# Performance work log

Measured on AMD Instinct MI355X. Metric: run time of the kernel, lower is better.

## Reference

```python
import jax, jax.numpy as jnp
import numpy as np

N, T, V, C = 16, 288, 25, 128
S, W = 8, 3            # num_subset, temporal window
IC = C // S            # inter_channels = 16
EPS = 1e-5


def _bn(x, g, b, m, v):
    # eval-mode BatchNorm2d over channel axis 1 of (N,C,T,V)
    inv = jax.lax.rsqrt(v + EPS)
    return (x - m[:, None, None]) * (inv * g)[:, None, None] + b[:, None, None]


def _conv1x1(x, w, b):
    # x: (N,Cin,T,V), w: (Cout,Cin), b: (Cout,)
    return jnp.einsum('nctv,oc->notv', x, w) + b[:, None, None]


def setup_inputs() -> dict:
    key = jax.random.key(0)
    ks = jax.random.split(key, 16)
    rn = lambda k, s, sc=0.05: jax.random.normal(k, s, dtype=jnp.float32) * sc
    inp = {
        'x': jax.random.normal(ks[0], (N, T, V, C), dtype=jnp.float32),
        'w_k': rn(ks[1], (S * IC, C)), 'b_k': rn(ks[2], (S * IC,)),
        'w_q': rn(ks[3], (S * IC, C)), 'b_q': rn(ks[4], (S * IC,)),
        'alphas': jnp.ones((1, S, 1, 1), jnp.float32),
        'att0': jnp.ones((1, S, W * V, V), jnp.float32) / V,
        'w_out': rn(ks[5], (C, S * C)), 'b_out': rn(ks[6], (C,)),
        'g_out': jnp.ones((C,), jnp.float32), 'beta_out': jnp.zeros((C,), jnp.float32),
        'm_out': jnp.zeros((C,), jnp.float32), 'v_out': jnp.ones((C,), jnp.float32),
        'w_ff': rn(ks[7], (C, C)), 'b_ff': rn(ks[8], (C,)),
        'g_ff': jnp.ones((C,), jnp.float32), 'beta_ff': jnp.zeros((C,), jnp.float32),
        'm_ff': jnp.zeros((C,), jnp.float32), 'v_ff': jnp.ones((C,), jnp.float32),
        'w_t': rn(ks[9], (C, C, 7, 1)), 'b_t': rn(ks[10], (C,)),
        'g_t': jnp.ones((C,), jnp.float32), 'beta_t': jnp.zeros((C,), jnp.float32),
        'm_t': jnp.zeros((C,), jnp.float32), 'v_t': jnp.ones((C,), jnp.float32),
    }
    return inp


def reference(x, w_k, b_k, w_q, b_q, alphas, att0,
              w_out, b_out, g_out, beta_out, m_out, v_out,
              w_ff, b_ff, g_ff, beta_ff, m_ff, v_ff,
              w_t, b_t, g_t, beta_t, m_t, v_t):
    leaky = lambda a: jax.nn.leaky_relu(a, 0.1)
    xc = jnp.transpose(x, (0, 3, 1, 2))                 # (N,C,T,V)
    # UnfoldTemporalWindows(window=3, stride=1, dilation=1, pad=1)
    xp = jnp.pad(xc, ((0, 0), (0, 0), (1, 1), (0, 0)))
    up = jnp.stack([xp[:, :, i:i + T] for i in range(W)], axis=3)   # (N,C,T,W,V)
    up = up.reshape(N, C, T, W * V)                      # (N,C,T,W*V)

    k = _conv1x1(xc, w_k, b_k).reshape(N, S, IC, T, V)
    q = _conv1x1(up, w_q, b_q).reshape(N, S, IC, T, W * V)
    scores = jnp.einsum('nsctu,nsctv->nsuv', q, k) / (IC * T)
    attention = jax.nn.softmax(scores, axis=-2) * alphas + att0      # atts buffer is zeros

    y = jnp.einsum('nctu,nsuv->nsctv', up, attention).reshape(N, S * C, T, V)
    y = _bn(_conv1x1(y, w_out, b_out), g_out, beta_out, m_out, v_out)
    y = leaky(xc + y)                                    # downs1 = identity (Cin==Cout)
    y = _bn(_conv1x1(y, w_ff, b_ff), g_ff, beta_ff, m_ff, v_ff)
    y = leaky(xc + y)                                    # downs2 = identity

    z = jax.lax.conv_general_dilated(
        y, w_t, window_strides=(1, 1), padding=((3, 3), (0, 0)),
        dimension_numbers=('NCHW', 'OIHW', 'NCHW')) + b_t[None, :, None, None]
    z = _bn(z, g_t, beta_t, m_t, v_t)
    z = leaky(y + z)                                     # downt2 = identity
    z = jax.nn.relu(z + xc)                              # residual add of identity
    return jnp.transpose(z, (0, 2, 3, 1))                # (N,T,V,C)
```

## Files before the change

### kernel.cpp

```cpp
#include <hip/hip_runtime.h>


#define NN 16
#define TT 288
#define VV 25
#define CC 128
#define SS 8
#define UU 75
#define TP 290
#define EPSF 1e-5f

typedef __attribute__((ext_vector_type(8))) short bf16x8;
typedef __attribute__((ext_vector_type(4))) float f32x4;

static __device__ __forceinline__ ushort f2bf(float f) {
  uint u = __float_as_uint(f);
  u = (u + 0x7FFFu + ((u >> 16) & 1u)) >> 16;
  return (ushort)u;
}

__global__ __launch_bounds__(256) void k_wcvt(
    const float* __restrict__ w_out, const float* __restrict__ w_k,
    const float* __restrict__ w_q, const float* __restrict__ w_ff,
    ushort* __restrict__ wb, ushort* __restrict__ wkqb,
    ushort* __restrict__ wffb) {
  int i = blockIdx.x * 256 + threadIdx.x;
  if (i < 131072) {
    int j = i >> 7, c = i & 127;
    int s = j >> 7, o = j & 127;
    wb[i] = f2bf(w_out[(o << 10) + (s << 7) + c]);
  } else {
    int j = i - 131072;
    if (j < 16384) wkqb[j] = f2bf(w_k[j]);
    else if (j < 32768) wkqb[j] = f2bf(w_q[j - 16384]);
    else wffb[j - 32768] = f2bf(w_ff[j - 32768]);
  }
}

__global__ __launch_bounds__(256) void k_qkg(
    const float* __restrict__ x, const ushort* __restrict__ wkqb,
    const float* __restrict__ b_k, const float* __restrict__ b_q,
    ushort* __restrict__ kb, ushort* __restrict__ qb) {
  __shared__ __align__(16) ushort As[8][128][8];
  __shared__ __align__(16) ushort Bs[8][128][8];
  const int bm = blockIdx.x, by = blockIdx.y;
  const int gm0 = bm << 7;
  const int tid = threadIdx.x;
  const int lane = tid & 63, wid = tid >> 6;
  const int wm = wid >> 1, wn = wid & 1;
  const int srow = tid & 127;
  const int skg0 = tid >> 7;
  const ushort* wsrc = wkqb + by * 16384;
  f32x4 acc[4][4] = {};
  for (int kh = 0; kh < 2; ++kh) {
    __syncthreads();
#pragma unroll
    for (int j = 0; j < 4; ++j) {
      int kg = skg0 + 2 * j;
      const float* xp = x + (((size_t)(gm0 + srow)) << 7) + kh * 64 + kg * 8;
      float4 a0 = *(const float4*)xp;
      float4 a1 = *(const float4*)(xp + 4);
      uint4 pk;
      pk.x = (uint)f2bf(a0.x) | ((uint)f2bf(a0.y) << 16);
      pk.y = (uint)f2bf(a0.z) | ((uint)f2bf(a0.w) << 16);
      pk.z = (uint)f2bf(a1.x) | ((uint)f2bf(a1.y) << 16);
      pk.w = (uint)f2bf(a1.z) | ((uint)f2bf(a1.w) << 16);
      *(uint4*)&As[kg][srow][0] = pk;
      *(uint4*)&Bs[kg][srow][0] =
          *(const uint4*)&wsrc[(srow << 7) + kh * 64 + kg * 8];
    }
    __syncthreads();
#pragma unroll
    for (int ks = 0; ks < 2; ++ks) {
      int g = ks * 4 + (lane >> 4);
      bf16x8 af[4], bfr[4];
#pragma unroll
      for (int mi = 0; mi < 4; ++mi)
        af[mi] = *(const bf16x8*)&As[g][wm * 64 + mi * 16 + (lane & 15)][0];
#pragma unroll
      for (int ni = 0; ni < 4; ++ni)
        bfr[ni] = *(const bf16x8*)&Bs[g][wn * 64 + ni * 16 + (lane & 15)][0];
#pragma unroll
      for (int mi = 0; mi < 4; ++mi)
#pragma unroll
        for (int ni = 0; ni < 4; ++ni)
          acc[mi][ni] = __builtin_amdgcn_mfma_f32_16x16x32_bf16(
              af[mi], bfr[ni], acc[mi][ni], 0, 0, 0);
    }
  }
  const int l15 = lane & 15, l4 = lane >> 4;
  const float* bias = by ? b_q : b_k;
#pragma unroll
  for (int ni = 0; ni < 4; ++ni) {
    int col = wn * 64 + ni * 16 + l15;
    float bb = bias[col];
#pragma unroll
    for (int mi = 0; mi < 4; ++mi) {
#pragma unroll
      for (int reg = 0; reg < 4; ++reg) {
        int row = gm0 + wm * 64 + mi * 16 + (l4 << 2) + reg;
        ushort val = f2bf(acc[mi][ni][reg] + bb);
        if (by == 0) {
          kb[((size_t)row << 7) + col] = val;
        } else {
          int n = row / 7200;
          qb[((size_t)(row + n * 50 + 25) << 7) + col] = val;
        }
      }
    }
  }
}

__global__ __launch_bounds__(256) void k_qkpad(const float* __restrict__ b_q,
                                               ushort* __restrict__ qb) {
  int i = blockIdx.x * 256 + threadIdx.x;
  int o = i & 127;
  int r = i >> 7;
  int v = r % 25;
  int e = (r / 25) & 1;
  int n = r / 50;
  int tp = e ? 289 : 0;
  qb[((size_t)((n * TP + tp) * VV + v) << 7) + o] = f2bf(b_q[o]);
}

__global__ __launch_bounds__(512) void k_scores(
    const ushort* __restrict__ kb, const ushort* __restrict__ qb,
    const float* __restrict__ alphas, const float* __restrict__ att0,
    ushort* __restrict__ attTb) {
  __shared__ float red[8][2640];
  __shared__ float scl[1875];
  __shared__ float mx[25];
  __shared__ float den[25];
  const int bx = blockIdx.x;
  const int n = bx >> 3, s = bx & 7;
  const int tid = threadIdx.x;
  const int lane = tid & 63, wid = tid >> 6;
  const int l15 = lane & 15, l4 = lane >> 4;
  const int dt = l4 >> 1;
  const int sic = s * 16 + (l4 & 1) * 8;
  int qoff[5];
#pragma unroll
  for (int tu = 0; tu < 5; ++tu) {
    int u = tu * 16 + l15;
    int w = u / 25, vp = u - w * 25;
    qoff[tu] = (w * 25 + vp) * 128 + sic;
  }
  const bool qv4 = (64 + l15) < 75;
  const bool kv1 = (16 + l15) < 25;
  int koff0 = l15 * 128 + sic;
  int koff1 = (16 + l15) * 128 + sic;
  const ushort* qbase = qb + (size_t)n * 928000 + (size_t)dt * 3200;
  const ushort* kbase = kb + (size_t)n * 921600 + (size_t)dt * 3200;
  f32x4 acc[5][2] = {};
  const bf16x8 zf = {};
  for (int kk = wid; kk < 144; kk += 8) {
    const ushort* qp = qbase + kk * 6400;
    const ushort* kp = kbase + kk * 6400;
    bf16x8 a[5], b[2];
#pragma unroll
    for (int tu = 0; tu < 4; ++tu) a[tu] = *(const bf16x8*)(qp + qoff[tu]);
    a[4] = qv4 ? *(const bf16x8*)(qp + qoff[4]) : zf;
    b[0] = *(const bf16x8*)(kp + koff0);
    b[1] = kv1 ? *(const bf16x8*)(kp + koff1) : zf;
#pragma unroll
    for (int tu = 0; tu < 5; ++tu)
#pragma unroll
      for (int tv = 0; tv < 2; ++tv)
        acc[tu][tv] = __builtin_amdgcn_mfma_f32_16x16x32_bf16(
            a[tu], b[tv], acc[tu][tv], 0, 0, 0);
  }
#pragma unroll
  for (int tu = 0; tu < 5; ++tu)
#pragma unroll
    for (int tv = 0; tv < 2; ++tv) {
#pragma unroll
      for (int reg = 0; reg < 4; ++reg)
        red[wid][(tu * 16 + l4 * 4 + reg) * 33 + tv * 16 + l15] =
            acc[tu][tv][reg];
    }
  __syncthreads();
  const float inv = 1.0f / 4608.0f;
  for (int i = tid; i < 1875; i += 512) {
    int u = i / 25, v = i - u * 25;
    float a = 0.f;
#pragma unroll
    for (int w = 0; w < 8; ++w) a += red[w][u * 33 + v];
    scl[i] = a * inv;
  }
  __syncthreads();
  if (tid < 25) {
    float m = -1e30f;
    for (int u = 0; u < 75; ++u) m = fmaxf(m, scl[u * 25 + tid]);
    float d = 0.f;
    for (int u = 0; u < 75; ++u) d += expf(scl[u * 25 + tid] - m);
    mx[tid] = m;
    den[tid] = d;
  }
  __syncthreads();
  const float alpha = alphas[s];
  ushort* op = attTb + (size_t)bx * 2400;
  for (int i = tid; i < 2400; i += 512) {
    int v = i / 96, u = i - v * 96;
    int w = u >> 5, vp = u & 31;
    float val = 0.f;
    if (vp < 25) {
      int uo = w * 25 + vp;
      val = expf(scl[uo * 25 + v] - mx[v]) / den[v] * alpha +
            att0[(s * 75 + uo) * 25 + v];
    }
    op[i] = f2bf(val);
  }
}

__global__ __launch_bounds__(256, 3) void k_attn3(
    const float* __restrict__ x, const ushort* __restrict__ attTb,
    const ushort* __restrict__ wb, const float* __restrict__ b_out,
    const float* __restrict__ g_out, const float* __restrict__ beta_out,
    const float* __restrict__ m_out, const float* __restrict__ v_out,
    float* __restrict__ y1) {
  __shared__ __align__(16) uint4 Xt4[128 * 16];
  __shared__ __align__(16) ushort Yl[2][32 * 136];
  const int t0 = blockIdx.x * 2, n = blockIdx.y;
  const int tid = threadIdx.x;
  for (int i = tid; i < 2048; i += 256) {
    int c = i & 127, chunk = i >> 7;
    int r = chunk >> 2, vp0 = (chunk & 3) * 8;
    int tr = t0 + r - 1;
    bool valid = (tr >= 0 && tr < TT);
    const float* xr = x + (((size_t)(n * TT + tr) * VV)) * 128 + c;
    float f[8];
#pragma unroll
    for (int j = 0; j < 8; ++j) {
      int vp = vp0 + j;
      f[j] = (valid && vp < 25) ? xr[vp * 128] : 0.f;
    }
    uint4 pk;
    pk.x = (uint)f2bf(f[0]) | ((uint)f2bf(f[1]) << 16);
    pk.y = (uint)f2bf(f[2]) | ((uint)f2bf(f[3]) << 16);
    pk.z = (uint)f2bf(f[4]) | ((uint)f2bf(f[5]) << 16);
    pk.w = (uint)f2bf(f[6]) | ((uint)f2bf(f[7]) << 16);
    Xt4[c * 16 + (chunk ^ (c & 7))] = pk;
  }
  __syncthreads();
  const int lane = tid & 63, wid = tid >> 6;
  const int l15 = lane & 15, l4 = lane >> 4;
  const bf16x8 zf = {};
  f32x4 accO[2][2][2] = {};
  const ushort* Avn = attTb + (size_t)n * 19200;
  const int c0r = wid * 32 + l15, c1r = wid * 32 + 16 + l15;
  for (int s = 0; s < 8; ++s) {
    const ushort* AvS = Avn + s * 2400;
    f32x4 accY[2][2][2] = {};
#pragma unroll
    for (int ks = 0; ks < 3; ++ks) {
      int u0 = ks * 32 + l4 * 8;
      bf16x8 av0 = *(const bf16x8*)&AvS[l15 * 96 + u0];
      int r1 = 16 + l15;
      bf16x8 av1 = *(const bf16x8*)&AvS[(r1 <= 24 ? r1 : 24) * 96 + u0];
      if (l15 > 8) av1 = zf;
#pragma unroll
      for (int tt = 0; tt < 2; ++tt) {
        int ch = (tt + ks) * 4 + l4;
        bf16x8 xb0 = *(const bf16x8*)&Xt4[c0r * 16 + (ch ^ (c0r & 7))];
        bf16x8 xb1 = *(const bf16x8*)&Xt4[c1r * 16 + (ch ^ (c1r & 7))];
        accY[tt][0][0] = __builtin_amdgcn_mfma_f32_16x16x32_bf16(av0, xb0, accY[tt][0][0], 0, 0, 0);
        accY[tt][0][1] = __builtin_amdgcn_mfma_f32_16x16x32_bf16(av0, xb1, accY[tt][0][1], 0, 0, 0);
        accY[tt][1][0] = __builtin_amdgcn_mfma_f32_16x16x32_bf16(av1, xb0, accY[tt][1][0], 0, 0, 0);
        accY[tt][1][1] = __builtin_amdgcn_mfma_f32_16x16x32_bf16(av1, xb1, accY[tt][1][1], 0, 0, 0);
      }
    }
    __syncthreads();
#pragma unroll
    for (int tt = 0; tt < 2; ++tt)
#pragma unroll
      for (int mi = 0; mi < 2; ++mi)
#pragma unroll
        for (int nj = 0; nj < 2; ++nj)
#pragma unroll
          for (int reg = 0; reg < 4; ++reg)
            Yl[tt][(mi * 16 + l4 * 4 + reg) * 136 + wid * 32 + nj * 16 + l15] =
                f2bf(accY[tt][mi][nj][reg]);
    __syncthreads();
    const ushort* wS = wb + s * 16384;
#pragma unroll
    for (int kc = 0; kc < 4; ++kc) {
      int c0 = kc * 32 + l4 * 8;
      bf16x8 wf0 = *(const bf16x8*)&wS[(wid * 32 + l15) * 128 + c0];
      bf16x8 wf1 = *(const bf16x8*)&wS[(wid * 32 + 16 + l15) * 128 + c0];
#pragma unroll
      for (int tt = 0; tt < 2; ++tt) {
        bf16x8 yb0 = *(const bf16x8*)&Yl[tt][l15 * 136 + c0];
        bf16x8 yb1 = *(const bf16x8*)&Yl[tt][(16 + l15) * 136 + c0];
        accO[tt][0][0] = __builtin_amdgcn_mfma_f32_16x16x32_bf16(wf0, yb0, accO[tt][0][0], 0, 0, 0);
        accO[tt][0][1] = __builtin_amdgcn_mfma_f32_16x16x32_bf16(wf0, yb1, accO[tt][0][1], 0, 0, 0);
        accO[tt][1][0] = __builtin_amdgcn_mfma_f32_16x16x32_bf16(wf1, yb0, accO[tt][1][0], 0, 0, 0);
        accO[tt][1][1] = __builtin_amdgcn_mfma_f32_16x16x32_bf16(wf1, yb1, accO[tt][1][1], 0, 0, 0);
      }
    }
  }
#pragma unroll
  for (int tt = 0; tt < 2; ++tt) {
    int t = t0 + tt;
#pragma unroll
    for (int nj = 0; nj < 2; ++nj) {
      int v = nj * 16 + l15;
      if (v < 25) {
        size_t rowbase = (((size_t)(n * TT + t) * VV + v)) * 128 + wid * 32;
#pragma unroll
        for (int mi = 0; mi < 2; ++mi) {
          int ob = mi * 16 + (l4 << 2);
          int og = wid * 32 + ob;
          float4 gg = *(const float4*)&g_out[og];
          float4 vv = *(const float4*)&v_out[og];
          float4 mm = *(const float4*)&m_out[og];
          float4 be = *(const float4*)&beta_out[og];
          float4 bo = *(const float4*)&b_out[og];
          float4 xv = *(const float4*)&x[rowbase + ob];
          float4 r;
          float s1, a;
          s1 = gg.x * rsqrtf(vv.x + EPSF);
          a = (accO[tt][mi][nj][0] + bo.x) * s1 + (be.x - mm.x * s1) + xv.x;
          r.x = a > 0.f ? a : 0.1f * a;
          s1 = gg.y * rsqrtf(vv.y + EPSF);
          a = (accO[tt][mi][nj][1] + bo.y) * s1 + (be.y - mm.y * s1) + xv.y;
          r.y = a > 0.f ? a : 0.1f * a;
          s1 = gg.z * rsqrtf(vv.z + EPSF);
          a = (accO[tt][mi][nj][2] + bo.z) * s1 + (be.z - mm.z * s1) + xv.z;
          r.z = a > 0.f ? a : 0.1f * a;
          s1 = gg.w * rsqrtf(vv.w + EPSF);
          a = (accO[tt][mi][nj][3] + bo.w) * s1 + (be.w - mm.w * s1) + xv.w;
          r.w = a > 0.f ? a : 0.1f * a;
          *(float4*)&y1[rowbase + ob] = r;
        }
      }
    }
  }
}

__global__ __launch_bounds__(256) void k_ffg(
    const float* __restrict__ y1, const float* __restrict__ x,
    const ushort* __restrict__ wffb, const float* __restrict__ b_ff,
    const float* __restrict__ g_ff, const float* __restrict__ beta_ff,
    const float* __restrict__ m_ff, const float* __restrict__ v_ff,
    float* __restrict__ y2) {
  __shared__ __align__(16) ushort As[8][128][8];
  __shared__ __align__(16) ushort Bs[8][128][8];
  const int gm0 = blockIdx.x << 7;
  const int tid = threadIdx.x;
  const int lane = tid & 63, wid = tid >> 6;
  const int wm = wid >> 1, wn = wid & 1;
  const int srow = tid & 127;
  const int skg0 = tid >> 7;
  f32x4 acc[4][4] = {};
  for (int kh = 0; kh < 2; ++kh) {
    __syncthreads();
#pragma unroll
    for (int j = 0; j < 4; ++j) {
      int kg = skg0 + 2 * j;
      const float* yp = y1 + (((size_t)(gm0 + srow)) << 7) + kh * 64 + kg * 8;
      float4 a0 = *(const float4*)yp;
      float4 a1 = *(const float4*)(yp + 4);
      uint4 pk;
      pk.x = (uint)f2bf(a0.x) | ((uint)f2bf(a0.y) << 16);
      pk.y = (uint)f2bf(a0.z) | ((uint)f2bf(a0.w) << 16);
      pk.z = (uint)f2bf(a1.x) | ((uint)f2bf(a1.y) << 16);
      pk.w = (uint)f2bf(a1.z) | ((uint)f2bf(a1.w) << 16);
      *(uint4*)&As[kg][srow][0] = pk;
      *(uint4*)&Bs[kg][srow][0] =
          *(const uint4*)&wffb[(srow << 7) + kh * 64 + kg * 8];
    }
    __syncthreads();
#pragma unroll
    for (int ks = 0; ks < 2; ++ks) {
      int g = ks * 4 + (lane >> 4);
      bf16x8 af[4], bfr[4];
#pragma unroll
      for (int mi = 0; mi < 4; ++mi)
        af[mi] = *(const bf16x8*)&As[g][wm * 64 + mi * 16 + (lane & 15)][0];
#pragma unroll
      for (int ni = 0; ni < 4; ++ni)
        bfr[ni] = *(const bf16x8*)&Bs[g][wn * 64 + ni * 16 + (lane & 15)][0];
#pragma unroll
      for (int mi = 0; mi < 4; ++mi)
#pragma unroll
        for (int ni = 0; ni < 4; ++ni)
          acc[mi][ni] = __builtin_amdgcn_mfma_f32_16x16x32_bf16(
              af[mi], bfr[ni], acc[mi][ni], 0, 0, 0);
    }
  }
  const int l15 = lane & 15, l4 = lane >> 4;
#pragma unroll
  for (int ni = 0; ni < 4; ++ni) {
    int o = wn * 64 + ni * 16 + l15;
    float s1 = g_ff[o] * rsqrtf(v_ff[o] + EPSF);
    float sh = beta_ff[o] - m_ff[o] * s1;
    float bb = b_ff[o];
#pragma unroll
    for (int mi = 0; mi < 4; ++mi) {
#pragma unroll
      for (int reg = 0; reg < 4; ++reg) {
        int row = gm0 + wm * 64 + mi * 16 + (l4 << 2) + reg;
        size_t idx = ((size_t)row << 7) + o;
        float a = (acc[mi][ni][reg] + bb) * s1 + sh;
        float rr = x[idx] + a;
        y2[idx] = rr > 0.f ? rr : 0.1f * rr;
      }
    }
  }
}

__global__ __launch_bounds__(256) void k_wtb(const float* __restrict__ w_t,
                                             ushort* __restrict__ wbt) {
  int i = blockIdx.x * 256 + threadIdx.x;
  if (i < 128 * 128 * 7) {
    int o = i / 896;
    int rem = i - o * 896;
    int c = rem / 7, kt = rem - c * 7;
    wbt[o * 896 + kt * 128 + c] = f2bf(w_t[i]);
  }
}

__global__ __launch_bounds__(256, 2) void k_tconv(
    const float* __restrict__ y2, const float* __restrict__ x,
    const ushort* __restrict__ wbt, const float* __restrict__ b_t,
    const float* __restrict__ g_t, const float* __restrict__ beta_t,
    const float* __restrict__ m_t, const float* __restrict__ v_t,
    float* __restrict__ out) {
  __shared__ __align__(16) uint4 As[280 * 16];
  const int n = blockIdx.y;
  const int r0 = blockIdx.x << 7;
  const int tid = threadIdx.x;
  const float* y2n = y2 + ((size_t)n * 7200 << 7);
  for (int i = tid; i < 278 * 16; i += 256) {
    int rl = i >> 4, cc = i & 15;
    int g = r0 - 75 + rl;
    uint4 pk = make_uint4(0u, 0u, 0u, 0u);
    if (g >= 0 && g < 7200) {
      const float* xp = y2n + ((size_t)g << 7) + (cc << 3);
      float4 a0 = *(const float4*)xp;
      float4 a1 = *(const float4*)(xp + 4);
      pk.x = (uint)f2bf(a0.x) | ((uint)f2bf(a0.y) << 16);
      pk.y = (uint)f2bf(a0.z) | ((uint)f2bf(a0.w) << 16);
      pk.z = (uint)f2bf(a1.x) | ((uint)f2bf(a1.y) << 16);
      pk.w = (uint)f2bf(a1.z) | ((uint)f2bf(a1.w) << 16);
    }
    As[(rl << 4) + (cc ^ (rl & 7))] = pk;
  }
  __syncthreads();
  const int lane = tid & 63, wid = tid >> 6;
  const int wm = wid >> 1, wn = wid & 1;
  const int l15 = lane & 15, l4 = lane >> 4;
  f32x4 acc[4][4] = {};
  for (int kt = 0; kt < 7; ++kt) {
    bf16x8 bfr[4][4];
#pragma unroll
    for (int ni = 0; ni < 4; ++ni) {
      const ushort* bp =
          wbt + (size_t)(wn * 64 + ni * 16 + l15) * 896 + kt * 128 + l4 * 8;
#pragma unroll
      for (int cc0 = 0; cc0 < 4; ++cc0)
        bfr[ni][cc0] = *(const bf16x8*)(bp + cc0 * 32);
    }
#pragma unroll
    for (int cc0 = 0; cc0 < 4; ++cc0) {
      bf16x8 af[4];
#pragma unroll
      for (int mi = 0; mi < 4; ++mi) {
        int rl = wm * 64 + mi * 16 + l15 + 25 * kt;
        af[mi] = *(const bf16x8*)&As[(rl << 4) + ((cc0 * 4 + l4) ^ (rl & 7))];
      }
#pragma unroll
      for (int mi = 0; mi < 4; ++mi)
#pragma unroll
        for (int ni = 0; ni < 4; ++ni)
          acc[mi][ni] = __builtin_amdgcn_mfma_f32_16x16x32_bf16(
              af[mi], bfr[ni][cc0], acc[mi][ni], 0, 0, 0);
    }
  }
#pragma unroll
  for (int ni = 0; ni < 4; ++ni) {
    int o = wn * 64 + ni * 16 + l15;
    float s1 = g_t[o] * rsqrtf(v_t[o] + EPSF);
    float sh = beta_t[o] - m_t[o] * s1;
    float bb = b_t[o];
#pragma unroll
    for (int mi = 0; mi < 4; ++mi) {
#pragma unroll
      for (int reg = 0; reg < 4; ++reg) {
        int grow = r0 + wm * 64 + mi * 16 + (l4 << 2) + reg;
        if (grow < 7200) {
          size_t idx = (((size_t)n * 7200 + grow) << 7) + o;
          float z = (acc[mi][ni][reg] + bb) * s1 + sh;
          z += y2[idx];
          z = z > 0.f ? z : 0.1f * z;
          z += x[idx];
          out[idx] = z > 0.f ? z : 0.f;
        }
      }
    }
  }
}

extern "C" void kernel_launch(void* const* d_in, const int* in_sizes, int n_in,
                              void* d_out, int out_size, void* d_ws, size_t ws_size,
                              hipStream_t stream) {
  const float* x      = (const float*)d_in[0];
  const float* w_k    = (const float*)d_in[1];
  const float* b_k    = (const float*)d_in[2];
  const float* w_q    = (const float*)d_in[3];
  const float* b_q    = (const float*)d_in[4];
  const float* alphas = (const float*)d_in[5];
  const float* att0   = (const float*)d_in[6];
  const float* w_out  = (const float*)d_in[7];
  const float* b_out  = (const float*)d_in[8];
  const float* g_out  = (const float*)d_in[9];
  const float* be_out = (const float*)d_in[10];
  const float* m_out  = (const float*)d_in[11];
  const float* v_out  = (const float*)d_in[12];
  const float* w_ff   = (const float*)d_in[13];
  const float* b_ff   = (const float*)d_in[14];
  const float* g_ff   = (const float*)d_in[15];
  const float* be_ff  = (const float*)d_in[16];
  const float* m_ff   = (const float*)d_in[17];
  const float* v_ff   = (const float*)d_in[18];
  const float* w_t    = (const float*)d_in[19];
  const float* b_t    = (const float*)d_in[20];
  const float* g_t    = (const float*)d_in[21];
  const float* be_t   = (const float*)d_in[22];
  const float* m_t    = (const float*)d_in[23];
  const float* v_t    = (const float*)d_in[24];

  float* ws = (float*)d_ws;
  float* qfull = ws;
  float* kfull = ws + 14848000;
  float* part  = ws + 29593600;
  float* attr  = ws + 31753600;
  float* wtr   = ws + 31993600;
  ushort* qbb   = (ushort*)qfull;
  ushort* kbb   = (ushort*)kfull;
  ushort* wb    = (ushort*)part;
  ushort* wkqb  = (ushort*)part + 131072;
  ushort* wffb  = (ushort*)part + 163840;
  ushort* attTb = (ushort*)attr;
  ushort* wbt   = (ushort*)wtr;
  float* y1 = kfull;
  float* y2 = qfull;
  float* outp = (float*)d_out;

  k_wcvt<<<704, 256, 0, stream>>>(w_out, w_k, w_q, w_ff, wb, wkqb, wffb);
  k_qkg<<<dim3(900, 2), 256, 0, stream>>>(x, wkqb, b_k, b_q, kbb, qbb);
  k_qkpad<<<400, 256, 0, stream>>>(b_q, qbb);
  k_scores<<<128, 512, 0, stream>>>(kbb, qbb, alphas, att0, attTb);
  k_attn3<<<dim3(144, 16), 256, 0, stream>>>(x, attTb, wb, b_out, g_out,
                                             be_out, m_out, v_out, y1);
  k_ffg<<<900, 256, 0, stream>>>(y1, x, wffb, b_ff, g_ff, be_ff, m_ff, v_ff, y2);
  k_wtb<<<448, 256, 0, stream>>>(w_t, wbt);
  k_tconv<<<dim3(57, 16), 256, 0, stream>>>(y2, x, wbt, b_t, g_t, be_t, m_t,
                                            v_t, outp);
}
```

Measured before the change: 400.5 us.

## Fuse feed-forward 1x1 conv into attention kernel epilogue and drop y1 round-trip

The attention/output-projection kernel now writes its leaky-relu result as bf16 into shared memory and immediately runs the 128x128 feed-forward 1x1 conv with MFMA, applying BN, the residual and leaky-relu before writing y2. This removes the separate k_ffg launch and the fp32 y1 write and re-read through global memory. The x tile layout in LDS also changes from an XOR-swizzled layout to a plain chunk-major layout. Costs include extra register pressure in a kernel already limited to 3 blocks per SM, and possible bank conflicts from dropping the swizzle.

```diff
diff --git a/kernel.cpp b/kernel.cpp
--- a/kernel.cpp
+++ b/kernel.cpp
@@ -217,8 +217,11 @@
     const ushort* __restrict__ wb, const float* __restrict__ b_out,
     const float* __restrict__ g_out, const float* __restrict__ beta_out,
     const float* __restrict__ m_out, const float* __restrict__ v_out,
-    float* __restrict__ y1) {
-  __shared__ __align__(16) uint4 Xt4[128 * 16];
+    const ushort* __restrict__ wffb, const float* __restrict__ b_ff,
+    const float* __restrict__ g_ff, const float* __restrict__ beta_ff,
+    const float* __restrict__ m_ff, const float* __restrict__ v_ff,
+    float* __restrict__ y2) {
+  __shared__ __align__(16) uint4 Xt4[16 * 128];
   __shared__ __align__(16) ushort Yl[2][32 * 136];
   const int t0 = blockIdx.x * 2, n = blockIdx.y;
   const int tid = threadIdx.x;
@@ -239,7 +242,7 @@
     pk.y = (uint)f2bf(f[2]) | ((uint)f2bf(f[3]) << 16);
     pk.z = (uint)f2bf(f[4]) | ((uint)f2bf(f[5]) << 16);
     pk.w = (uint)f2bf(f[6]) | ((uint)f2bf(f[7]) << 16);
-    Xt4[c * 16 + (chunk ^ (c & 7))] = pk;
+    Xt4[chunk * 128 + c] = pk;
   }
   __syncthreads();
   const int lane = tid & 63, wid = tid >> 6;
@@ -261,8 +264,8 @@
 #pragma unroll
       for (int tt = 0; tt < 2; ++tt) {
         int ch = (tt + ks) * 4 + l4;
-        bf16x8 xb0 = *(const bf16x8*)&Xt4[c0r * 16 + (ch ^ (c0r & 7))];
-        bf16x8 xb1 = *(const bf16x8*)&Xt4[c1r * 16 + (ch ^ (c1r & 7))];
+        bf16x8 xb0 = *(const bf16x8*)&Xt4[ch * 128 + c0r];
+        bf16x8 xb1 = *(const bf16x8*)&Xt4[ch * 128 + c1r];
         accY[tt][0][0] = __builtin_amdgcn_mfma_f32_16x16x32_bf16(av0, xb0, accY[tt][0][0], 0, 0, 0);
         accY[tt][0][1] = __builtin_amdgcn_mfma_f32_16x16x32_bf16(av0, xb1, accY[tt][0][1], 0, 0, 0);
         accY[tt][1][0] = __builtin_amdgcn_mfma_f32_16x16x32_bf16(av1, xb0, accY[tt][1][0], 0, 0, 0);
@@ -298,12 +301,14 @@
       }
     }
   }
+  __syncthreads();
 #pragma unroll
   for (int tt = 0; tt < 2; ++tt) {
     int t = t0 + tt;
 #pragma unroll
     for (int nj = 0; nj < 2; ++nj) {
       int v = nj * 16 + l15;
+      ushort pv[2][4];
       if (v < 25) {
         size_t rowbase = (((size_t)(n * TT + t) * VV + v)) * 128 + wid * 32;
 #pragma unroll
@@ -316,94 +321,84 @@
           float4 be = *(const float4*)&beta_out[og];
           float4 bo = *(const float4*)&b_out[og];
           float4 xv = *(const float4*)&x[rowbase + ob];
+          float s1, a;
+          s1 = gg.x * rsqrtf(vv.x + EPSF);
+          a = (accO[tt][mi][nj][0] + bo.x) * s1 + (be.x - mm.x * s1) + xv.x;
+          pv[mi][0] = f2bf(a > 0.f ? a : 0.1f * a);
+          s1 = gg.y * rsqrtf(vv.y + EPSF);
+          a = (accO[tt][mi][nj][1] + bo.y) * s1 + (be.y - mm.y * s1) + xv.y;
+          pv[mi][1] = f2bf(a > 0.f ? a : 0.1f * a);
+          s1 = gg.z * rsqrtf(vv.z + EPSF);
+          a = (accO[tt][mi][nj][2] + bo.z) * s1 + (be.z - mm.z * s1) + xv.z;
+          pv[mi][2] = f2bf(a > 0.f ? a : 0.1f * a);
+          s1 = gg.w * rsqrtf(vv.w + EPSF);
+          a = (accO[tt][mi][nj][3] + bo.w) * s1 + (be.w - mm.w * s1) + xv.w;
+          pv[mi][3] = f2bf(a > 0.f ? a : 0.1f * a);
+        }
+      } else {
+#pragma unroll
+        for (int mi = 0; mi < 2; ++mi)
+#pragma unroll
+          for (int reg = 0; reg < 4; ++reg) pv[mi][reg] = 0;
+      }
+#pragma unroll
+      for (int mi = 0; mi < 2; ++mi)
+#pragma unroll
+        for (int reg = 0; reg < 4; ++reg)
+          Yl[tt][v * 136 + wid * 32 + mi * 16 + (l4 << 2) + reg] = pv[mi][reg];
+    }
+  }
+  __syncthreads();
+  f32x4 accF[2][2][2] = {};
+#pragma unroll
+  for (int kc = 0; kc < 4; ++kc) {
+    int c0 = kc * 32 + l4 * 8;
+    bf16x8 wf0 = *(const bf16x8*)&wffb[(wid * 32 + l15) * 128 + c0];
+    bf16x8 wf1 = *(const bf16x8*)&wffb[(wid * 32 + 16 + l15) * 128 + c0];
+#pragma unroll
+    for (int tt = 0; tt < 2; ++tt) {
+      bf16x8 yb0 = *(const bf16x8*)&Yl[tt][l15 * 136 + c0];
+      bf16x8 yb1 = *(const bf16x8*)&Yl[tt][(16 + l15) * 136 + c0];
+      accF[tt][0][0] = __builtin_amdgcn_mfma_f32_16x16x32_bf16(wf0, yb0, accF[tt][0][0], 0, 0, 0);
+      accF[tt][0][1] = __builtin_amdgcn_mfma_f32_16x16x32_bf16(wf0, yb1, accF[tt][0][1], 0, 0, 0);
+      accF[tt][1][0] = __builtin_amdgcn_mfma_f32_16x16x32_bf16(wf1, yb0, accF[tt][1][0], 0, 0, 0);
+      accF[tt][1][1] = __builtin_amdgcn_mfma_f32_16x16x32_bf16(wf1, yb1, accF[tt][1][1], 0, 0, 0);
+    }
+  }
+#pragma unroll
+  for (int tt = 0; tt < 2; ++tt) {
+    int t = t0 + tt;
+#pragma unroll
+    for (int nj = 0; nj < 2; ++nj) {
+      int v = nj * 16 + l15;
+      if (v < 25) {
+        size_t rowbase = (((size_t)(n * TT + t) * VV + v)) * 128 + wid * 32;
+#pragma unroll
+        for (int mi = 0; mi < 2; ++mi) {
+          int ob = mi * 16 + (l4 << 2);
+          int og = wid * 32 + ob;
+          float4 gg = *(const float4*)&g_ff[og];
+          float4 vv = *(const float4*)&v_ff[og];
+          float4 mm = *(const float4*)&m_ff[og];
+          float4 be = *(const float4*)&beta_ff[og];
+          float4 bo = *(const float4*)&b_ff[og];
+          float4 xv = *(const float4*)&x[rowbase + ob];
           float4 r;
           float s1, a;
           s1 = gg.x * rsqrtf(vv.x + EPSF);
-          a = (accO[tt][mi][nj][0] + bo.x) * s1 + (be.x - mm.x * s1) + xv.x;
+          a = (accF[tt][mi][nj][0] + bo.x) * s1 + (be.x - mm.x * s1) + xv.x;
           r.x = a > 0.f ? a : 0.1f * a;
           s1 = gg.y * rsqrtf(vv.y + EPSF);
-          a = (accO[tt][mi][nj][1] + bo.y) * s1 + (be.y - mm.y * s1) + xv.y;
+          a = (accF[tt][mi][nj][1] + bo.y) * s1 + (be.y - mm.y * s1) + xv.y;
           r.y = a > 0.f ? a : 0.1f * a;
           s1 = gg.z * rsqrtf(vv.z + EPSF);
-          a = (accO[tt][mi][nj][2] + bo.z) * s1 + (be.z - mm.z * s1) + xv.z;
+          a = (accF[tt][mi][nj][2] + bo.z) * s1 + (be.z - mm.z * s1) + xv.z;
           r.z = a > 0.f ? a : 0.1f * a;
           s1 = gg.w * rsqrtf(vv.w + EPSF);
-          a = (accO[tt][mi][nj][3] + bo.w) * s1 + (be.w - mm.w * s1) + xv.w;
+          a = (accF[tt][mi][nj][3] + bo.w) * s1 + (be.w - mm.w * s1) + xv.w;
           r.w = a > 0.f ? a : 0.1f * a;
-          *(float4*)&y1[rowbase + ob] = r;
+          *(float4*)&y2[rowbase + ob] = r;
         }
-      }
-    }
-  }
-}
-
-__global__ __launch_bounds__(256) void k_ffg(
-    const float* __restrict__ y1, const float* __restrict__ x,
-    const ushort* __restrict__ wffb, const float* __restrict__ b_ff,
-    const float* __restrict__ g_ff, const float* __restrict__ beta_ff,
-    const float* __restrict__ m_ff, const float* __restrict__ v_ff,
-    float* __restrict__ y2) {
-  __shared__ __align__(16) ushort As[8][128][8];
-  __shared__ __align__(16) ushort Bs[8][128][8];
-  const int gm0 = blockIdx.x << 7;
-  const int tid = threadIdx.x;
-  const int lane = tid & 63, wid = tid >> 6;
-  const int wm = wid >> 1, wn = wid & 1;
-  const int srow = tid & 127;
-  const int skg0 = tid >> 7;
-  f32x4 acc[4][4] = {};
-  for (int kh = 0; kh < 2; ++kh) {
-    __syncthreads();
-#pragma unroll
-    for (int j = 0; j < 4; ++j) {
-      int kg = skg0 + 2 * j;
-      const float* yp = y1 + (((size_t)(gm0 + srow)) << 7) + kh * 64 + kg * 8;
-      float4 a0 = *(const float4*)yp;
-      float4 a1 = *(const float4*)(yp + 4);
-      uint4 pk;
-      pk.x = (uint)f2bf(a0.x) | ((uint)f2bf(a0.y) << 16);
-      pk.y = (uint)f2bf(a0.z) | ((uint)f2bf(a0.w) << 16);
-      pk.z = (uint)f2bf(a1.x) | ((uint)f2bf(a1.y) << 16);
-      pk.w = (uint)f2bf(a1.z) | ((uint)f2bf(a1.w) << 16);
-      *(uint4*)&As[kg][srow][0] = pk;
-      *(uint4*)&Bs[kg][srow][0] =
-          *(const uint4*)&wffb[(srow << 7) + kh * 64 + kg * 8];
-    }
-    __syncthreads();
-#pragma unroll
-    for (int ks = 0; ks < 2; ++ks) {
-      int g = ks * 4 + (lane >> 4);
-      bf16x8 af[4], bfr[4];
-#pragma unroll
-      for (int mi = 0; mi < 4; ++mi)
-        af[mi] = *(const bf16x8*)&As[g][wm * 64 + mi * 16 + (lane & 15)][0];
-#pragma unroll
-      for (int ni = 0; ni < 4; ++ni)
-        bfr[ni] = *(const bf16x8*)&Bs[g][wn * 64 + ni * 16 + (lane & 15)][0];
-#pragma unroll
-      for (int mi = 0; mi < 4; ++mi)
-#pragma unroll
-        for (int ni = 0; ni < 4; ++ni)
-          acc[mi][ni] = __builtin_amdgcn_mfma_f32_16x16x32_bf16(
-              af[mi], bfr[ni], acc[mi][ni], 0, 0, 0);
-    }
-  }
-  const int l15 = lane & 15, l4 = lane >> 4;
-#pragma unroll
-  for (int ni = 0; ni < 4; ++ni) {
-    int o = wn * 64 + ni * 16 + l15;
-    float s1 = g_ff[o] * rsqrtf(v_ff[o] + EPSF);
-    float sh = beta_ff[o] - m_ff[o] * s1;
-    float bb = b_ff[o];
-#pragma unroll
-    for (int mi = 0; mi < 4; ++mi) {
-#pragma unroll
-      for (int reg = 0; reg < 4; ++reg) {
-        int row = gm0 + wm * 64 + mi * 16 + (l4 << 2) + reg;
-        size_t idx = ((size_t)row << 7) + o;
-        float a = (acc[mi][ni][reg] + bb) * s1 + sh;
-        float rr = x[idx] + a;
-        y2[idx] = rr > 0.f ? rr : 0.1f * rr;
       }
     }
   }
@@ -543,7 +538,6 @@
   ushort* wffb  = (ushort*)part + 163840;
   ushort* attTb = (ushort*)attr;
   ushort* wbt   = (ushort*)wtr;
-  float* y1 = kfull;
   float* y2 = qfull;
   float* outp = (float*)d_out;
 
@@ -552,8 +546,8 @@
   k_qkpad<<<400, 256, 0, stream>>>(b_q, qbb);
   k_scores<<<128, 512, 0, stream>>>(kbb, qbb, alphas, att0, attTb);
   k_attn3<<<dim3(144, 16), 256, 0, stream>>>(x, attTb, wb, b_out, g_out,
-                                             be_out, m_out, v_out, y1);
-  k_ffg<<<900, 256, 0, stream>>>(y1, x, wffb, b_ff, g_ff, be_ff, m_ff, v_ff, y2);
+                                             be_out, m_out, v_out, wffb, b_ff,
+                                             g_ff, be_ff, m_ff, v_ff, y2);
   k_wtb<<<448, 256, 0, stream>>>(w_t, wbt);
   k_tconv<<<dim3(57, 16), 256, 0, stream>>>(y2, x, wbt, b_t, g_t, be_t, m_t,
                                             v_t, outp);
```

Result: faster. 376.6 us (-6.0%).
